# Kernel optimization log

Measured on AMD Instinct MI355X. Metric: run time of the kernel, lower is better.

Reference implementation:

```python
import jax
import jax.numpy as jnp
import numpy as np

B, R, C, Q, D = 16, 2048, 81, 65, 1024
K = 1024          # pre-NMS candidate cap (fixed-shape stand-in for torch's dynamic filtering)
DET = 100         # detections_per_img
IMG = 640.0       # square image size (clip bound)
SCORE_THRESH = 0.05
NMS_THRESH = 0.5
MIN_SIZE = 0.01
BBOX_CLIP = float(np.log(1000.0 / 16.0))  # torchvision BoxCoder bbox_xform_clip
WX, WY, WW, WH = 10.0, 10.0, 5.0, 5.0     # BoxCoder weights


def setup_inputs() -> dict:
    key = jax.random.key(0)
    k1, k2, k3, k4, k5, k6 = jax.random.split(key, 6)
    class_logits = 2.0 * jax.random.normal(k1, (B, R, C), jnp.float32)
    quantity_logits = jax.random.normal(k2, (B, R, Q), jnp.float32)
    box_features = jax.random.normal(k3, (B, R, D), jnp.float32)
    box_regression = 0.5 * jax.random.normal(k4, (B, R, C * 4), jnp.float32)
    cxcy = jax.random.uniform(k5, (B, R, 2), jnp.float32, 0.0, IMG)
    wh = jax.random.uniform(k6, (B, R, 2), jnp.float32, 10.0, 80.0)
    x1y1 = jnp.clip(cxcy - 0.5 * wh, 0.0, IMG)
    x2y2 = jnp.clip(cxcy + 0.5 * wh, 0.0, IMG)
    proposals = jnp.concatenate([x1y1, x2y2], axis=-1)
    return {
        'class_logits': class_logits,
        'quantity_logits': quantity_logits,
        'box_features': box_features,
        'box_regression': box_regression,
        'proposals': proposals,
    }


def _decode(deltas, props):
    # deltas: [R, C, 4], props: [R, 4] -> boxes [R, C, 4] (torchvision BoxCoder.decode)
    pw = props[:, 2] - props[:, 0]
    ph = props[:, 3] - props[:, 1]
    pcx = props[:, 0] + 0.5 * pw
    pcy = props[:, 1] + 0.5 * ph
    dx = deltas[..., 0] / WX
    dy = deltas[..., 1] / WY
    dw = jnp.minimum(deltas[..., 2] / WW, BBOX_CLIP)
    dh = jnp.minimum(deltas[..., 3] / WH, BBOX_CLIP)
    cx = dx * pw[:, None] + pcx[:, None]
    cy = dy * ph[:, None] + pcy[:, None]
    w = jnp.exp(dw) * pw[:, None]
    h = jnp.exp(dh) * ph[:, None]
    return jnp.stack([cx - 0.5 * w, cy - 0.5 * h, cx + 0.5 * w, cy + 0.5 * h], axis=-1)


def _iou_matrix(b):
    # b: [K, 4] -> pairwise IoU [K, K]
    area = (b[:, 2] - b[:, 0]) * (b[:, 3] - b[:, 1])
    lt = jnp.maximum(b[:, None, :2], b[None, :, :2])
    rb = jnp.minimum(b[:, None, 2:], b[None, :, 2:])
    whv = jnp.clip(rb - lt, 0.0)
    inter = whv[..., 0] * whv[..., 1]
    return inter / (area[:, None] + area[None, :] - inter + 1e-9)


def _process_image(logits, qlogits, feats, reg, props):
    # decode + clip
    boxes = jnp.clip(_decode(reg.reshape(R, C, 4), props), 0.0, IMG)  # [R, C, 4]
    scores = jax.nn.softmax(logits, axis=-1)                          # [R, C]
    quant = jnp.argmax(qlogits, axis=-1).astype(jnp.int32)            # [R]
    # drop background class 0, flatten to M = R*(C-1)
    fb = boxes[:, 1:, :].reshape(-1, 4)
    fs = scores[:, 1:].reshape(-1)
    fl = jnp.broadcast_to(jnp.arange(1, C, dtype=jnp.int32), (R, C - 1)).reshape(-1)
    fi = jnp.broadcast_to(jnp.arange(R, dtype=jnp.int32)[:, None], (R, C - 1)).reshape(-1)
    bw = fb[:, 2] - fb[:, 0]
    bh = fb[:, 3] - fb[:, 1]
    valid = (fs > SCORE_THRESH) & (bw >= MIN_SIZE) & (bh >= MIN_SIZE)
    # top-K candidates by masked score (sorted desc)
    top_s, top_i = jax.lax.top_k(jnp.where(valid, fs, -1.0), K)
    cb = fb[top_i]          # [K, 4]
    cl = fl[top_i]          # [K]
    ci = fi[top_i]          # [K] row index into proposals/features
    cv = top_s > 0.0        # candidate validity (score_thresh > 0)
    # batched NMS via per-class coordinate offset
    ob = cb + (cl.astype(jnp.float32) * (IMG + 1.0))[:, None]
    iou = _iou_matrix(ob)
    ar = jnp.arange(K)

    def body(i, keep):
        sup = (iou[i] > NMS_THRESH) & (ar > i)
        return jnp.where(keep[i] & cv[i], keep & ~sup, keep)

    keep = jax.lax.fori_loop(0, K, body, cv) & cv
    # first DET survivors in score order
    det_s, det_i = jax.lax.top_k(jnp.where(keep, top_s, -1.0), DET)
    dv = det_s > 0.0
    m = dv.astype(jnp.float32)
    db = cb[det_i] * m[:, None]
    dl = jnp.where(dv, cl[det_i], 0)
    di = ci[det_i]
    dq = jnp.where(dv, quant[di], 0)
    df = feats[di] * m[:, None]   # irregular gather of box features by surviving row idx
    ds = jnp.where(dv, det_s, 0.0)
    return db, ds, dl, dq, df, dv


def reference(class_logits, quantity_logits, box_features, box_regression, proposals):
    # returns (boxes [B,DET,4], scores [B,DET], labels [B,DET] i32,
    #          quantities [B,DET] i32, features [B,DET,D], valid [B,DET] bool)
    return jax.vmap(_process_image)(class_logits, quantity_logits, box_features,
                                    box_regression, proposals)
```

## Files before the change

### kernel.cpp

```cpp
#include <hip/hip_runtime.h>
#include <math.h>

#define NB 16
#define NR 2048
#define NC 81
#define NQ 65
#define ND 1024
#define NK 1024
#define NDET 100
#define NBLK 512
#define BSLOT 64
#define HBINS 5184
#define CH 256
#define L2CAP 384
#define LRCAP 1536
#define BBC 4.135166556742356f

#define O_BOX   0
#define O_SCORE (NB*NDET*4)
#define O_LABEL (O_SCORE + NB*NDET)
#define O_QUANT (O_LABEL + NB*NDET)
#define O_FEAT  (O_QUANT + NB*NDET)
#define O_VALID (O_FEAT + (size_t)NB*NDET*ND)

#define WS_CAND  ((size_t)0)
#define WS_GHIST (WS_CAND + (size_t)NB*NBLK*BSLOT*8)
#define WS_DETCB (WS_GHIST + (size_t)NB*HBINS*4)
#define WS_DETM  (WS_DETCB + (size_t)NB*NDET*16)
#define WS_DETS  (WS_DETM + (size_t)NB*NDET*4)
#define WS_CNT   (WS_DETS + (size_t)NB*NDET*4)

__device__ __forceinline__ float4 decode_box(float4 d, float pw, float ph,
                                             float pcx, float pcy) {
    float dx = d.x / 10.0f, dy = d.y / 10.0f;
    float dw = fminf(d.z / 5.0f, BBC), dh = fminf(d.w / 5.0f, BBC);
    float cx = dx * pw + pcx, cy = dy * ph + pcy;
    float w = expf(dw) * pw, h = expf(dh) * ph;
    float4 r;
    r.x = fminf(fmaxf(cx - 0.5f * w, 0.0f), 640.0f);
    r.y = fminf(fmaxf(cy - 0.5f * h, 0.0f), 640.0f);
    r.z = fminf(fmaxf(cx + 0.5f * w, 0.0f), 640.0f);
    r.w = fminf(fmaxf(cy + 0.5f * h, 0.0f), 640.0f);
    return r;
}

__global__ __launch_bounds__(256) void k_stage1(
    const float* __restrict__ logits, const float* __restrict__ reg,
    const float* __restrict__ props, unsigned long long* __restrict__ cand,
    int* __restrict__ cnt, unsigned int* __restrict__ ghist) {
    __shared__ unsigned long long sl[BSLOT];
    __shared__ int scnt;
    int b = blockIdx.x >> 9;
    int blk = blockIdx.x & (NBLK - 1);
    int wid = threadIdx.x >> 6;
    int lane = threadIdx.x & 63;
    int r = blk * 4 + wid;
    int row = b * NR + r;
    if (threadIdx.x == 0) scnt = 0;
    __syncthreads();

    const float* Lrow = logits + (size_t)row * NC;
    float v0 = Lrow[lane];
    float v1 = (lane < NC - 64) ? Lrow[64 + lane] : -1e30f;
    float mx = fmaxf(v0, v1);
    #pragma unroll
    for (int o = 32; o; o >>= 1) mx = fmaxf(mx, __shfl_xor(mx, o));
    float e = expf(v0 - mx) + ((lane < NC - 64) ? expf(v1 - mx) : 0.0f);
    float sm = e;
    #pragma unroll
    for (int o = 32; o; o >>= 1) sm += __shfl_xor(sm, o);
    float thr_lo = mx + logf(0.05f * sm) - 0.01f;

    const float* P = props + (size_t)row * 4;
    float p0 = P[0], p1 = P[1], p2 = P[2], p3 = P[3];
    float pw = p2 - p0, ph = p3 - p1;
    float pcx = p0 + 0.5f * pw, pcy = p1 + 0.5f * ph;
    const float* G = reg + (size_t)row * (NC * 4);

    #pragma unroll
    for (int pass = 0; pass < 2; ++pass) {
        int cc = lane + pass * 64;
        if (cc < NC - 1) {
            int c = cc + 1;
            float lc = Lrow[c];
            if (lc > thr_lo) {
                float p = expf(lc - mx) / sm;
                float4 d = *(const float4*)(G + 4 * c);
                float4 bx = decode_box(d, pw, ph, pcx, pcy);
                float bw = bx.z - bx.x, bh = bx.w - bx.y;
                if (p > 0.05f && bw >= 0.01f && bh >= 0.01f) {
                    int m = r * 80 + cc;
                    int pos = atomicAdd(&scnt, 1);
                    if (pos < BSLOT) {
                        sl[pos] = ((unsigned long long)__float_as_uint(p) << 32) |
                                  (unsigned)(~(unsigned)m);
                        unsigned bin = (__float_as_uint(p) - 0x3D000000u) >> 13;
                        atomicAdd(&ghist[b * HBINS + bin], 1u);
                    }
                }
            }
        }
    }
    __syncthreads();
    int n = scnt < BSLOT ? scnt : BSLOT;
    unsigned long long* dst = cand + ((size_t)b * NBLK + blk) * BSLOT;
    for (int i = threadIdx.x; i < n; i += 256) dst[i] = sl[i];
    if (threadIdx.x == 0) cnt[b * NBLK + blk] = n;
}

__global__ __launch_bounds__(1024) void k_fused(
    const unsigned long long* __restrict__ cand, const int* __restrict__ cnt,
    const unsigned int* __restrict__ ghist,
    const float* __restrict__ reg, const float* __restrict__ props,
    int* __restrict__ det_m, float* __restrict__ det_s,
    float4* __restrict__ det_cb) {
    __shared__ union {
        unsigned int hist[HBINS];
        unsigned long long sortedRest[LRCAP];
    } u;
    __shared__ unsigned long long list2[L2CAP], sorted2[L2CAP];
    __shared__ unsigned long long listRest[LRCAP];
    __shared__ float4 boff[L2CAP], bclip[L2CAP];
    __shared__ int scn[NBLK];
    __shared__ int s_c2, s_cR, s_b1, s_b2, s_A, s_need;
    int b = blockIdx.x, tid = threadIdx.x;
    const unsigned long long* cnd = cand + (size_t)b * NBLK * BSLOT;

    for (int i = tid; i < HBINS; i += 1024) u.hist[i] = ghist[b * HBINS + i];
    if (tid < NBLK) scn[tid] = cnt[b * NBLK + tid];
    if (tid == 0) { s_c2 = 0; s_cR = 0; s_b1 = 0; s_b2 = 0; s_A = 0; s_need = 0; }
    __syncthreads();

    if (tid < 64) {
        int lane = tid, base = lane * 81;
        unsigned partial = 0;
        for (int j = 0; j < 81; ++j) partial += u.hist[base + j];
        unsigned incl = partial;
        #pragma unroll
        for (int o = 1; o < 64; o <<= 1) {
            unsigned t = __shfl_up(incl, o);
            if (lane >= o) incl += t;
        }
        unsigned total = __shfl(incl, 63);
        unsigned suffix = total - incl;
        if (suffix < NK && suffix + partial >= NK) {
            unsigned A = suffix;
            for (int bb = base + 80; bb >= base; --bb) {
                unsigned An = A + u.hist[bb];
                if (An >= NK) { s_b1 = bb; break; }
                A = An;
            }
        }
        if (suffix < CH && suffix + partial >= CH) {
            unsigned A = suffix;
            for (int bb = base + 80; bb >= base; --bb) {
                unsigned An = A + u.hist[bb];
                if (An >= CH) { s_b2 = bb; break; }
                A = An;
            }
        }
    }
    __syncthreads();
    int b1 = s_b1, b2 = s_b2;

    for (int i = tid; i < NBLK * BSLOT; i += 1024) {
        if ((i & (BSLOT - 1)) < scn[i >> 6]) {
            unsigned long long key = cnd[i];
            int bin = (int)(((unsigned)(key >> 32) - 0x3D000000u) >> 13);
            if (bin >= b2) {
                int p = atomicAdd(&s_c2, 1);
                if (p < L2CAP) list2[p] = key;
            } else if (bin >= b1) {
                int p = atomicAdd(&s_cR, 1);
                if (p < LRCAP) listRest[p] = key;
            }
        }
    }
    __syncthreads();
    int T2 = s_c2 < L2CAP ? s_c2 : L2CAP;
    int TR = s_cR < LRCAP ? s_cR : LRCAP;
    int S = T2 + TR;
    int cap = S < NK ? S : NK;
    int limit1 = T2 < cap ? T2 : cap;

    if (tid < T2) {
        unsigned long long k0 = list2[tid];
        int rk = 0;
        for (int j = 0; j < T2; ++j) rk += (list2[j] > k0);
        sorted2[rk] = k0;
    }
    __syncthreads();

    if (tid < limit1) {
        unsigned long long key = sorted2[tid];
        int m = (int)(~(unsigned)key);
        int r = m / 80, c = m - r * 80 + 1;
        size_t row = (size_t)b * NR + r;
        float4 P = *(const float4*)(props + row * 4);
        float pw = P.z - P.x, ph = P.w - P.y;
        float pcx = P.x + 0.5f * pw, pcy = P.y + 0.5f * ph;
        float4 d = *(const float4*)(reg + row * (NC * 4) + 4 * c);
        float4 bx = decode_box(d, pw, ph, pcx, pcy);
        bclip[tid] = bx;
        float off = (float)c * 641.0f;
        float4 o = {bx.x + off, bx.y + off, bx.z + off, bx.w + off};
        boff[tid] = o;
    }
    __syncthreads();

    int lane = tid & 63;
    float4 a0 = {0, 0, 0, 0}, a1 = {0, 0, 0, 0};
    int A = 0;
    if (tid < 64) {
        unsigned long long nk_ = (limit1 > 0) ? sorted2[0] : 0ull;
        float4 nb_ = (limit1 > 0) ? boff[0] : a0;
        for (int t = 0; t < limit1; ++t) {
            unsigned long long keyt = nk_;
            float4 bt = nb_;
            if (t + 1 < limit1) { nk_ = sorted2[t + 1]; nb_ = boff[t + 1]; }
            float areaB = (bt.z - bt.x) * (bt.w - bt.y);
            float areaA0 = (a0.z - a0.x) * (a0.w - a0.y);
            float ltx = fmaxf(a0.x, bt.x), lty = fmaxf(a0.y, bt.y);
            float rbx = fminf(a0.z, bt.z), rby = fminf(a0.w, bt.w);
            float in0 = fmaxf(rbx - ltx, 0.0f) * fmaxf(rby - lty, 0.0f);
            bool sup = (lane < A) && (in0 / (areaA0 + areaB - in0 + 1e-9f) > 0.5f);
            if (A > 64) {
                float areaA1 = (a1.z - a1.x) * (a1.w - a1.y);
                float l1 = fmaxf(a1.x, bt.x), t1 = fmaxf(a1.y, bt.y);
                float r1 = fminf(a1.z, bt.z), b1f = fminf(a1.w, bt.w);
                float in1 = fmaxf(r1 - l1, 0.0f) * fmaxf(b1f - t1, 0.0f);
                sup |= (lane + 64 < A) &&
                       (in1 / (areaA1 + areaB - in1 + 1e-9f) > 0.5f);
            }
            if (!__any((int)sup)) {
                if (lane == (A & 63)) { if (A < 64) a0 = bt; else a1 = bt; }
                if (lane == 0) {
                    det_m[b * NDET + A] = (int)(~(unsigned)keyt);
                    det_s[b * NDET + A] = __uint_as_float((unsigned)(keyt >> 32));
                    det_cb[b * NDET + A] = bclip[t];
                }
                ++A;
                if (A == NDET) break;
            }
        }
        if (tid == 0) { s_A = A; s_need = (A < NDET && limit1 < cap) ? 1 : 0; }
    }
    __syncthreads();

    if (s_need) {
        for (int t0 = tid; t0 < TR; t0 += 1024) {
            unsigned long long k0 = listRest[t0];
            int rk = 0;
            for (int j = 0; j < TR; ++j) rk += (listRest[j] > k0);
            u.sortedRest[rk] = k0;
        }
        __syncthreads();
        if (tid < 64) {
            int nrest = cap - limit1;
            for (int t = 0; t < nrest && A < NDET; ++t) {
                unsigned long long keyt = u.sortedRest[t];
                int m = (int)(~(unsigned)keyt);
                int r = m / 80, c = m - r * 80 + 1;
                size_t row = (size_t)b * NR + r;
                float4 P = *(const float4*)(props + row * 4);
                float pw = P.z - P.x, ph = P.w - P.y;
                float pcx = P.x + 0.5f * pw, pcy = P.y + 0.5f * ph;
                float4 d = *(const float4*)(reg + row * (NC * 4) + 4 * c);
                float4 bx = decode_box(d, pw, ph, pcx, pcy);
                float off = (float)c * 641.0f;
                float4 bt = {bx.x + off, bx.y + off, bx.z + off, bx.w + off};
                float areaB = (bt.z - bt.x) * (bt.w - bt.y);
                float areaA0 = (a0.z - a0.x) * (a0.w - a0.y);
                float ltx = fmaxf(a0.x, bt.x), lty = fmaxf(a0.y, bt.y);
                float rbx = fminf(a0.z, bt.z), rby = fminf(a0.w, bt.w);
                float in0 = fmaxf(rbx - ltx, 0.0f) * fmaxf(rby - lty, 0.0f);
                bool sup = (lane < A) &&
                           (in0 / (areaA0 + areaB - in0 + 1e-9f) > 0.5f);
                if (A > 64) {
                    float areaA1 = (a1.z - a1.x) * (a1.w - a1.y);
                    float l1 = fmaxf(a1.x, bt.x), t1 = fmaxf(a1.y, bt.y);
                    float r1 = fminf(a1.z, bt.z), b1f = fminf(a1.w, bt.w);
                    float in1 = fmaxf(r1 - l1, 0.0f) * fmaxf(b1f - t1, 0.0f);
                    sup |= (lane + 64 < A) &&
                           (in1 / (areaA1 + areaB - in1 + 1e-9f) > 0.5f);
                }
                if (!__any((int)sup)) {
                    if (lane == (A & 63)) { if (A < 64) a0 = bt; else a1 = bt; }
                    if (lane == 0) {
                        det_m[b * NDET + A] = m;
                        det_s[b * NDET + A] =
                            __uint_as_float((unsigned)(keyt >> 32));
                        det_cb[b * NDET + A] = bx;
                    }
                    ++A;
                }
            }
            if (tid == 0) s_A = A;
        }
        __syncthreads();
    }
    for (int d = s_A + tid; d < NDET; d += 1024) det_m[b * NDET + d] = -1;
}

__global__ __launch_bounds__(256) void k_final(
    const float* __restrict__ feats, const float* __restrict__ qlog,
    const int* __restrict__ det_m, const float* __restrict__ det_s,
    const float4* __restrict__ det_cb, float* __restrict__ out) {
    int bd = blockIdx.x;
    int b = bd / NDET;
    int t = threadIdx.x;
    int m = det_m[bd];
    float4* of = (float4*)(out + O_FEAT + (size_t)bd * ND);
    if (m >= 0) {
        int r = m / 80, c = m - r * 80 + 1;
        size_t row = (size_t)b * NR + r;
        if (t == 0) {
            ((float4*)(out + O_BOX))[bd] = det_cb[bd];
            out[O_SCORE + bd] = det_s[bd];
            out[O_LABEL + bd] = (float)c;
            out[O_VALID + bd] = 1.0f;
        }
        if (t < 64) {
            const float* Qrow = qlog + row * NQ;
            float qv = Qrow[t];
            int qi = t;
            if (t == 0) {
                float q64 = Qrow[64];
                if (q64 > qv) { qv = q64; qi = 64; }
            }
            #pragma unroll
            for (int o = 32; o; o >>= 1) {
                float ov = __shfl_xor(qv, o);
                int oi = __shfl_xor(qi, o);
                if (ov > qv || (ov == qv && oi < qi)) { qv = ov; qi = oi; }
            }
            if (t == 0) out[O_QUANT + bd] = (float)qi;
        }
        const float4* f = (const float4*)(feats + row * ND);
        of[t] = f[t];
    } else {
        if (t == 0) {
            float4 z = {0, 0, 0, 0};
            ((float4*)(out + O_BOX))[bd] = z;
            out[O_SCORE + bd] = 0.0f;
            out[O_LABEL + bd] = 0.0f;
            out[O_QUANT + bd] = 0.0f;
            out[O_VALID + bd] = 0.0f;
        }
        float4 z = {0, 0, 0, 0};
        of[t] = z;
    }
}

extern "C" void kernel_launch(void* const* d_in, const int* in_sizes, int n_in,
                              void* d_out, int out_size, void* d_ws, size_t ws_size,
                              hipStream_t stream) {
    const float* logits = (const float*)d_in[0];
    const float* qlog   = (const float*)d_in[1];
    const float* feats  = (const float*)d_in[2];
    const float* reg    = (const float*)d_in[3];
    const float* props  = (const float*)d_in[4];
    float* out = (float*)d_out;
    char* ws = (char*)d_ws;

    unsigned long long* cand = (unsigned long long*)(ws + WS_CAND);
    unsigned int* ghist = (unsigned int*)(ws + WS_GHIST);
    float4* det_cb = (float4*)(ws + WS_DETCB);
    int* det_m = (int*)(ws + WS_DETM);
    float* det_s = (float*)(ws + WS_DETS);
    int* cnt = (int*)(ws + WS_CNT);

    hipMemsetAsync(ghist, 0, (size_t)NB * HBINS * 4, stream);
    k_stage1<<<NB * NBLK, 256, 0, stream>>>(logits, reg, props, cand, cnt, ghist);
    k_fused<<<NB, 1024, 0, stream>>>(cand, cnt, ghist, reg, props, det_m, det_s,
                                     det_cb);
    k_final<<<NB * NDET, 256, 0, stream>>>(feats, qlog, det_m, det_s, det_cb, out);
}
```

Baseline: 294.8 us.

## Fuse all stages into one cooperative persistent kernel with grid syncs

Replaces the memset plus three kernel launches with a single cooperative kernel of 512 blocks that uses grid.sync between histogram clearing, candidate scoring, per-image NMS and output gathering. Stage 1 now assigns 16 rows per wave and compacts candidates with ballot/popcount into per-wave slots instead of shared-memory atomics. The aim is to remove launch and inter-kernel gaps. In exchange, the NMS stage runs on only 16 blocks of 256 threads, down from 1024, while the other blocks sit idle at a grid barrier, and the scoring phase has less parallelism.

```diff
diff --git a/kernel.cpp b/kernel.cpp
--- a/kernel.cpp
+++ b/kernel.cpp
@@ -1,5 +1,8 @@
 #include <hip/hip_runtime.h>
+#include <hip/hip_cooperative_groups.h>
 #include <math.h>
+
+namespace cg = cooperative_groups;
 
 #define NB 16
 #define NR 2048
@@ -8,8 +11,11 @@
 #define ND 1024
 #define NK 1024
 #define NDET 100
-#define NBLK 512
-#define BSLOT 64
+#define GRID 512
+#define NWAVE 2048
+#define WPI 128
+#define RPW 16
+#define WSLOT 128
 #define HBINS 5184
 #define CH 256
 #define L2CAP 384
@@ -24,11 +30,11 @@
 #define O_VALID (O_FEAT + (size_t)NB*NDET*ND)
 
 #define WS_CAND  ((size_t)0)
-#define WS_GHIST (WS_CAND + (size_t)NB*NBLK*BSLOT*8)
-#define WS_DETCB (WS_GHIST + (size_t)NB*HBINS*4)
-#define WS_DETM  (WS_DETCB + (size_t)NB*NDET*16)
+#define WS_GHIST (WS_CAND + (size_t)NWAVE*WSLOT*8)
+#define WS_CNT   (WS_GHIST + (size_t)NB*HBINS*4)
+#define WS_DETM  (WS_CNT + (size_t)NWAVE*4)
 #define WS_DETS  (WS_DETM + (size_t)NB*NDET*4)
-#define WS_CNT   (WS_DETS + (size_t)NB*NDET*4)
+#define WS_DETCB (WS_DETS + (size_t)NB*NDET*4)
 
 __device__ __forceinline__ float4 decode_box(float4 d, float pw, float ph,
                                              float pcx, float pcy) {
@@ -44,231 +50,191 @@
     return r;
 }
 
-__global__ __launch_bounds__(256) void k_stage1(
-    const float* __restrict__ logits, const float* __restrict__ reg,
-    const float* __restrict__ props, unsigned long long* __restrict__ cand,
-    int* __restrict__ cnt, unsigned int* __restrict__ ghist) {
-    __shared__ unsigned long long sl[BSLOT];
-    __shared__ int scnt;
-    int b = blockIdx.x >> 9;
-    int blk = blockIdx.x & (NBLK - 1);
-    int wid = threadIdx.x >> 6;
-    int lane = threadIdx.x & 63;
-    int r = blk * 4 + wid;
-    int row = b * NR + r;
-    if (threadIdx.x == 0) scnt = 0;
-    __syncthreads();
-
-    const float* Lrow = logits + (size_t)row * NC;
-    float v0 = Lrow[lane];
-    float v1 = (lane < NC - 64) ? Lrow[64 + lane] : -1e30f;
-    float mx = fmaxf(v0, v1);
-    #pragma unroll
-    for (int o = 32; o; o >>= 1) mx = fmaxf(mx, __shfl_xor(mx, o));
-    float e = expf(v0 - mx) + ((lane < NC - 64) ? expf(v1 - mx) : 0.0f);
-    float sm = e;
-    #pragma unroll
-    for (int o = 32; o; o >>= 1) sm += __shfl_xor(sm, o);
-    float thr_lo = mx + logf(0.05f * sm) - 0.01f;
-
-    const float* P = props + (size_t)row * 4;
-    float p0 = P[0], p1 = P[1], p2 = P[2], p3 = P[3];
-    float pw = p2 - p0, ph = p3 - p1;
-    float pcx = p0 + 0.5f * pw, pcy = p1 + 0.5f * ph;
-    const float* G = reg + (size_t)row * (NC * 4);
-
-    #pragma unroll
-    for (int pass = 0; pass < 2; ++pass) {
-        int cc = lane + pass * 64;
-        if (cc < NC - 1) {
-            int c = cc + 1;
-            float lc = Lrow[c];
-            if (lc > thr_lo) {
-                float p = expf(lc - mx) / sm;
-                float4 d = *(const float4*)(G + 4 * c);
-                float4 bx = decode_box(d, pw, ph, pcx, pcy);
-                float bw = bx.z - bx.x, bh = bx.w - bx.y;
-                if (p > 0.05f && bw >= 0.01f && bh >= 0.01f) {
-                    int m = r * 80 + cc;
-                    int pos = atomicAdd(&scnt, 1);
-                    if (pos < BSLOT) {
-                        sl[pos] = ((unsigned long long)__float_as_uint(p) << 32) |
-                                  (unsigned)(~(unsigned)m);
-                        unsigned bin = (__float_as_uint(p) - 0x3D000000u) >> 13;
-                        atomicAdd(&ghist[b * HBINS + bin], 1u);
-                    }
-                }
-            }
-        }
-    }
-    __syncthreads();
-    int n = scnt < BSLOT ? scnt : BSLOT;
-    unsigned long long* dst = cand + ((size_t)b * NBLK + blk) * BSLOT;
-    for (int i = threadIdx.x; i < n; i += 256) dst[i] = sl[i];
-    if (threadIdx.x == 0) cnt[b * NBLK + blk] = n;
-}
-
-__global__ __launch_bounds__(1024) void k_fused(
-    const unsigned long long* __restrict__ cand, const int* __restrict__ cnt,
-    const unsigned int* __restrict__ ghist,
-    const float* __restrict__ reg, const float* __restrict__ props,
-    int* __restrict__ det_m, float* __restrict__ det_s,
-    float4* __restrict__ det_cb) {
-    __shared__ union {
+struct SharedB {
+    union {
         unsigned int hist[HBINS];
         unsigned long long sortedRest[LRCAP];
     } u;
-    __shared__ unsigned long long list2[L2CAP], sorted2[L2CAP];
-    __shared__ unsigned long long listRest[LRCAP];
-    __shared__ float4 boff[L2CAP], bclip[L2CAP];
-    __shared__ int scn[NBLK];
-    __shared__ int s_c2, s_cR, s_b1, s_b2, s_A, s_need;
-    int b = blockIdx.x, tid = threadIdx.x;
-    const unsigned long long* cnd = cand + (size_t)b * NBLK * BSLOT;
-
-    for (int i = tid; i < HBINS; i += 1024) u.hist[i] = ghist[b * HBINS + i];
-    if (tid < NBLK) scn[tid] = cnt[b * NBLK + tid];
-    if (tid == 0) { s_c2 = 0; s_cR = 0; s_b1 = 0; s_b2 = 0; s_A = 0; s_need = 0; }
-    __syncthreads();
-
-    if (tid < 64) {
-        int lane = tid, base = lane * 81;
-        unsigned partial = 0;
-        for (int j = 0; j < 81; ++j) partial += u.hist[base + j];
-        unsigned incl = partial;
-        #pragma unroll
-        for (int o = 1; o < 64; o <<= 1) {
-            unsigned t = __shfl_up(incl, o);
-            if (lane >= o) incl += t;
-        }
-        unsigned total = __shfl(incl, 63);
-        unsigned suffix = total - incl;
-        if (suffix < NK && suffix + partial >= NK) {
-            unsigned A = suffix;
-            for (int bb = base + 80; bb >= base; --bb) {
-                unsigned An = A + u.hist[bb];
-                if (An >= NK) { s_b1 = bb; break; }
-                A = An;
-            }
-        }
-        if (suffix < CH && suffix + partial >= CH) {
-            unsigned A = suffix;
-            for (int bb = base + 80; bb >= base; --bb) {
-                unsigned An = A + u.hist[bb];
-                if (An >= CH) { s_b2 = bb; break; }
-                A = An;
-            }
-        }
+    unsigned long long list2[L2CAP], sorted2[L2CAP], listRest[LRCAP];
+    float4 boff[L2CAP], bclip[L2CAP];
+    int scn[WPI];
+    int s_c2, s_cR, s_b1, s_b2, s_A, s_need;
+};
+
+__global__ __launch_bounds__(256, 2) void k_all(
+    const float* __restrict__ logits, const float* __restrict__ qlog,
+    const float* __restrict__ feats, const float* __restrict__ reg,
+    const float* __restrict__ props, unsigned long long* __restrict__ cand,
+    unsigned int* __restrict__ ghist, int* __restrict__ cnt,
+    int* __restrict__ det_m, float* __restrict__ det_s,
+    float4* __restrict__ det_cb, float* __restrict__ out) {
+    cg::grid_group grid = cg::this_grid();
+    __shared__ SharedB sb;
+    int tid = threadIdx.x;
+    int lane = tid & 63;
+
+    for (int i = blockIdx.x * 256 + tid; i < NB * HBINS; i += GRID * 256)
+        ghist[i] = 0;
+    grid.sync();
+
+    {
+        int W = blockIdx.x * 4 + (tid >> 6);
+        int b = W >> 7, wi = W & (WPI - 1);
+        unsigned long long* wreg = cand + (size_t)W * WSLOT;
+        int cur = 0;
+        for (int t = 0; t < RPW; ++t) {
+            int r = wi * RPW + t;
+            int row = b * NR + r;
+            const float* Lrow = logits + (size_t)row * NC;
+            float v0 = Lrow[lane];
+            float v1 = (lane < NC - 64) ? Lrow[64 + lane] : -1e30f;
+            float mx = fmaxf(v0, v1);
+            #pragma unroll
+            for (int o = 32; o; o >>= 1) mx = fmaxf(mx, __shfl_xor(mx, o));
+            float e = expf(v0 - mx) + ((lane < NC - 64) ? expf(v1 - mx) : 0.0f);
+            float sm = e;
+            #pragma unroll
+            for (int o = 32; o; o >>= 1) sm += __shfl_xor(sm, o);
+            float thr_lo = mx + logf(0.05f * sm) - 0.01f;
+
+            float4 P = *(const float4*)(props + (size_t)row * 4);
+            float pw = P.z - P.x, ph = P.w - P.y;
+            float pcx = P.x + 0.5f * pw, pcy = P.y + 0.5f * ph;
+            const float* G = reg + (size_t)row * (NC * 4);
+
+            #pragma unroll
+            for (int pass = 0; pass < 2; ++pass) {
+                int cc = lane + pass * 64;
+                bool ok = false;
+                unsigned long long key = 0;
+                if (cc < NC - 1) {
+                    int c = cc + 1;
+                    float lc = Lrow[c];
+                    if (lc > thr_lo) {
+                        float p = expf(lc - mx) / sm;
+                        float4 d = *(const float4*)(G + 4 * c);
+                        float4 bx = decode_box(d, pw, ph, pcx, pcy);
+                        float bw = bx.z - bx.x, bh = bx.w - bx.y;
+                        if (p > 0.05f && bw >= 0.01f && bh >= 0.01f) {
+                            ok = true;
+                            unsigned m = (unsigned)(r * 80 + cc);
+                            key = ((unsigned long long)__float_as_uint(p) << 32) |
+                                  (unsigned)(~m);
+                        }
+                    }
+                }
+                unsigned long long msk = __ballot(ok);
+                int rk = __popcll(msk & ((1ull << lane) - 1ull));
+                if (ok && cur + rk < WSLOT) {
+                    wreg[cur + rk] = key;
+                    unsigned bin = ((unsigned)(key >> 32) - 0x3D000000u) >> 13;
+                    atomicAdd(&ghist[b * HBINS + bin], 1u);
+                }
+                cur += (int)__popcll(msk);
+            }
+        }
+        if (lane == 0) cnt[W] = cur < WSLOT ? cur : WSLOT;
     }
-    __syncthreads();
-    int b1 = s_b1, b2 = s_b2;
-
-    for (int i = tid; i < NBLK * BSLOT; i += 1024) {
-        if ((i & (BSLOT - 1)) < scn[i >> 6]) {
-            unsigned long long key = cnd[i];
-            int bin = (int)(((unsigned)(key >> 32) - 0x3D000000u) >> 13);
-            if (bin >= b2) {
-                int p = atomicAdd(&s_c2, 1);
-                if (p < L2CAP) list2[p] = key;
-            } else if (bin >= b1) {
-                int p = atomicAdd(&s_cR, 1);
-                if (p < LRCAP) listRest[p] = key;
-            }
-        }
-    }
-    __syncthreads();
-    int T2 = s_c2 < L2CAP ? s_c2 : L2CAP;
-    int TR = s_cR < LRCAP ? s_cR : LRCAP;
-    int S = T2 + TR;
-    int cap = S < NK ? S : NK;
-    int limit1 = T2 < cap ? T2 : cap;
-
-    if (tid < T2) {
-        unsigned long long k0 = list2[tid];
-        int rk = 0;
-        for (int j = 0; j < T2; ++j) rk += (list2[j] > k0);
-        sorted2[rk] = k0;
-    }
-    __syncthreads();
-
-    if (tid < limit1) {
-        unsigned long long key = sorted2[tid];
-        int m = (int)(~(unsigned)key);
-        int r = m / 80, c = m - r * 80 + 1;
-        size_t row = (size_t)b * NR + r;
-        float4 P = *(const float4*)(props + row * 4);
-        float pw = P.z - P.x, ph = P.w - P.y;
-        float pcx = P.x + 0.5f * pw, pcy = P.y + 0.5f * ph;
-        float4 d = *(const float4*)(reg + row * (NC * 4) + 4 * c);
-        float4 bx = decode_box(d, pw, ph, pcx, pcy);
-        bclip[tid] = bx;
-        float off = (float)c * 641.0f;
-        float4 o = {bx.x + off, bx.y + off, bx.z + off, bx.w + off};
-        boff[tid] = o;
-    }
-    __syncthreads();
-
-    int lane = tid & 63;
-    float4 a0 = {0, 0, 0, 0}, a1 = {0, 0, 0, 0};
-    int A = 0;
-    if (tid < 64) {
-        unsigned long long nk_ = (limit1 > 0) ? sorted2[0] : 0ull;
-        float4 nb_ = (limit1 > 0) ? boff[0] : a0;
-        for (int t = 0; t < limit1; ++t) {
-            unsigned long long keyt = nk_;
-            float4 bt = nb_;
-            if (t + 1 < limit1) { nk_ = sorted2[t + 1]; nb_ = boff[t + 1]; }
-            float areaB = (bt.z - bt.x) * (bt.w - bt.y);
-            float areaA0 = (a0.z - a0.x) * (a0.w - a0.y);
-            float ltx = fmaxf(a0.x, bt.x), lty = fmaxf(a0.y, bt.y);
-            float rbx = fminf(a0.z, bt.z), rby = fminf(a0.w, bt.w);
-            float in0 = fmaxf(rbx - ltx, 0.0f) * fmaxf(rby - lty, 0.0f);
-            bool sup = (lane < A) && (in0 / (areaA0 + areaB - in0 + 1e-9f) > 0.5f);
-            if (A > 64) {
-                float areaA1 = (a1.z - a1.x) * (a1.w - a1.y);
-                float l1 = fmaxf(a1.x, bt.x), t1 = fmaxf(a1.y, bt.y);
-                float r1 = fminf(a1.z, bt.z), b1f = fminf(a1.w, bt.w);
-                float in1 = fmaxf(r1 - l1, 0.0f) * fmaxf(b1f - t1, 0.0f);
-                sup |= (lane + 64 < A) &&
-                       (in1 / (areaA1 + areaB - in1 + 1e-9f) > 0.5f);
-            }
-            if (!__any((int)sup)) {
-                if (lane == (A & 63)) { if (A < 64) a0 = bt; else a1 = bt; }
-                if (lane == 0) {
-                    det_m[b * NDET + A] = (int)(~(unsigned)keyt);
-                    det_s[b * NDET + A] = __uint_as_float((unsigned)(keyt >> 32));
-                    det_cb[b * NDET + A] = bclip[t];
-                }
-                ++A;
-                if (A == NDET) break;
-            }
-        }
-        if (tid == 0) { s_A = A; s_need = (A < NDET && limit1 < cap) ? 1 : 0; }
-    }
-    __syncthreads();
-
-    if (s_need) {
-        for (int t0 = tid; t0 < TR; t0 += 1024) {
-            unsigned long long k0 = listRest[t0];
+    grid.sync();
+
+    if (blockIdx.x < NB) {
+        int b = blockIdx.x;
+        const unsigned long long* cnd = cand + (size_t)b * WPI * WSLOT;
+
+        for (int i = tid; i < HBINS; i += 256) sb.u.hist[i] = ghist[b * HBINS + i];
+        if (tid < WPI) sb.scn[tid] = cnt[b * WPI + tid];
+        if (tid == 0) {
+            sb.s_c2 = 0; sb.s_cR = 0; sb.s_b1 = 0; sb.s_b2 = 0;
+            sb.s_A = 0; sb.s_need = 0;
+        }
+        __syncthreads();
+
+        if (tid < 64) {
+            int base = lane * 81;
+            unsigned partial = 0;
+            for (int j = 0; j < 81; ++j) partial += sb.u.hist[base + j];
+            unsigned incl = partial;
+            #pragma unroll
+            for (int o = 1; o < 64; o <<= 1) {
+                unsigned t = __shfl_up(incl, o);
+                if (lane >= o) incl += t;
+            }
+            unsigned total = __shfl(incl, 63);
+            unsigned suffix = total - incl;
+            if (suffix < NK && suffix + partial >= NK) {
+                unsigned A = suffix;
+                for (int bb = base + 80; bb >= base; --bb) {
+                    unsigned An = A + sb.u.hist[bb];
+                    if (An >= NK) { sb.s_b1 = bb; break; }
+                    A = An;
+                }
+            }
+            if (suffix < CH && suffix + partial >= CH) {
+                unsigned A = suffix;
+                for (int bb = base + 80; bb >= base; --bb) {
+                    unsigned An = A + sb.u.hist[bb];
+                    if (An >= CH) { sb.s_b2 = bb; break; }
+                    A = An;
+                }
+            }
+        }
+        __syncthreads();
+        int b1 = sb.s_b1, b2 = sb.s_b2;
+
+        for (int i = tid; i < WPI * WSLOT; i += 256) {
+            if ((i & (WSLOT - 1)) < sb.scn[i >> 7]) {
+                unsigned long long key = cnd[i];
+                int bin = (int)(((unsigned)(key >> 32) - 0x3D000000u) >> 13);
+                if (bin >= b2) {
+                    int p = atomicAdd(&sb.s_c2, 1);
+                    if (p < L2CAP) sb.list2[p] = key;
+                } else if (bin >= b1) {
+                    int p = atomicAdd(&sb.s_cR, 1);
+                    if (p < LRCAP) sb.listRest[p] = key;
+                }
+            }
+        }
+        __syncthreads();
+        int T2 = sb.s_c2 < L2CAP ? sb.s_c2 : L2CAP;
+        int TR = sb.s_cR < LRCAP ? sb.s_cR : LRCAP;
+        int S = T2 + TR;
+        int cap = S < NK ? S : NK;
+        int limit1 = T2 < cap ? T2 : cap;
+
+        for (int t0 = tid; t0 < T2; t0 += 256) {
+            unsigned long long k0 = sb.list2[t0];
             int rk = 0;
-            for (int j = 0; j < TR; ++j) rk += (listRest[j] > k0);
-            u.sortedRest[rk] = k0;
-        }
-        __syncthreads();
+            for (int j = 0; j < T2; ++j) rk += (sb.list2[j] > k0);
+            sb.sorted2[rk] = k0;
+        }
+        __syncthreads();
+
+        for (int t0 = tid; t0 < limit1; t0 += 256) {
+            unsigned long long key = sb.sorted2[t0];
+            int m = (int)(~(unsigned)key);
+            int r = m / 80, c = m - r * 80 + 1;
+            size_t row = (size_t)b * NR + r;
+            float4 P = *(const float4*)(props + row * 4);
+            float pw = P.z - P.x, ph = P.w - P.y;
+            float pcx = P.x + 0.5f * pw, pcy = P.y + 0.5f * ph;
+            float4 d = *(const float4*)(reg + row * (NC * 4) + 4 * c);
+            float4 bx = decode_box(d, pw, ph, pcx, pcy);
+            sb.bclip[t0] = bx;
+            float off = (float)c * 641.0f;
+            float4 o = {bx.x + off, bx.y + off, bx.z + off, bx.w + off};
+            sb.boff[t0] = o;
+        }
+        __syncthreads();
+
+        float4 a0 = {0, 0, 0, 0}, a1 = {0, 0, 0, 0};
+        int A = 0;
         if (tid < 64) {
-            int nrest = cap - limit1;
-            for (int t = 0; t < nrest && A < NDET; ++t) {
-                unsigned long long keyt = u.sortedRest[t];
-                int m = (int)(~(unsigned)keyt);
-                int r = m / 80, c = m - r * 80 + 1;
-                size_t row = (size_t)b * NR + r;
-                float4 P = *(const float4*)(props + row * 4);
-                float pw = P.z - P.x, ph = P.w - P.y;
-                float pcx = P.x + 0.5f * pw, pcy = P.y + 0.5f * ph;
-                float4 d = *(const float4*)(reg + row * (NC * 4) + 4 * c);
-                float4 bx = decode_box(d, pw, ph, pcx, pcy);
-                float off = (float)c * 641.0f;
-                float4 bt = {bx.x + off, bx.y + off, bx.z + off, bx.w + off};
+            unsigned long long nk_ = (limit1 > 0) ? sb.sorted2[0] : 0ull;
+            float4 nb_ = (limit1 > 0) ? sb.boff[0] : a0;
+            for (int t = 0; t < limit1; ++t) {
+                unsigned long long keyt = nk_;
+                float4 bt = nb_;
+                if (t + 1 < limit1) { nk_ = sb.sorted2[t + 1]; nb_ = sb.boff[t + 1]; }
                 float areaB = (bt.z - bt.x) * (bt.w - bt.y);
                 float areaA0 = (a0.z - a0.x) * (a0.w - a0.y);
                 float ltx = fmaxf(a0.x, bt.x), lty = fmaxf(a0.y, bt.y);
@@ -287,68 +253,121 @@
                 if (!__any((int)sup)) {
                     if (lane == (A & 63)) { if (A < 64) a0 = bt; else a1 = bt; }
                     if (lane == 0) {
-                        det_m[b * NDET + A] = m;
+                        det_m[b * NDET + A] = (int)(~(unsigned)keyt);
                         det_s[b * NDET + A] =
                             __uint_as_float((unsigned)(keyt >> 32));
-                        det_cb[b * NDET + A] = bx;
+                        det_cb[b * NDET + A] = sb.bclip[t];
                     }
                     ++A;
-                }
-            }
-            if (tid == 0) s_A = A;
-        }
-        __syncthreads();
+                    if (A == NDET) break;
+                }
+            }
+            if (tid == 0) {
+                sb.s_A = A;
+                sb.s_need = (A < NDET && limit1 < cap) ? 1 : 0;
+            }
+        }
+        __syncthreads();
+
+        if (sb.s_need) {
+            for (int t0 = tid; t0 < TR; t0 += 256) {
+                unsigned long long k0 = sb.listRest[t0];
+                int rk = 0;
+                for (int j = 0; j < TR; ++j) rk += (sb.listRest[j] > k0);
+                sb.u.sortedRest[rk] = k0;
+            }
+            __syncthreads();
+            if (tid < 64) {
+                int nrest = cap - limit1;
+                for (int t = 0; t < nrest && A < NDET; ++t) {
+                    unsigned long long keyt = sb.u.sortedRest[t];
+                    int m = (int)(~(unsigned)keyt);
+                    int r = m / 80, c = m - r * 80 + 1;
+                    size_t row = (size_t)b * NR + r;
+                    float4 P = *(const float4*)(props + row * 4);
+                    float pw = P.z - P.x, ph = P.w - P.y;
+                    float pcx = P.x + 0.5f * pw, pcy = P.y + 0.5f * ph;
+                    float4 d = *(const float4*)(reg + row * (NC * 4) + 4 * c);
+                    float4 bx = decode_box(d, pw, ph, pcx, pcy);
+                    float off = (float)c * 641.0f;
+                    float4 bt = {bx.x + off, bx.y + off, bx.z + off, bx.w + off};
+                    float areaB = (bt.z - bt.x) * (bt.w - bt.y);
+                    float areaA0 = (a0.z - a0.x) * (a0.w - a0.y);
+                    float ltx = fmaxf(a0.x, bt.x), lty = fmaxf(a0.y, bt.y);
+                    float rbx = fminf(a0.z, bt.z), rby = fminf(a0.w, bt.w);
+                    float in0 = fmaxf(rbx - ltx, 0.0f) * fmaxf(rby - lty, 0.0f);
+                    bool sup = (lane < A) &&
+                               (in0 / (areaA0 + areaB - in0 + 1e-9f) > 0.5f);
+                    if (A > 64) {
+                        float areaA1 = (a1.z - a1.x) * (a1.w - a1.y);
+                        float l1 = fmaxf(a1.x, bt.x), t1 = fmaxf(a1.y, bt.y);
+                        float r1 = fminf(a1.z, bt.z), b1f = fminf(a1.w, bt.w);
+                        float in1 = fmaxf(r1 - l1, 0.0f) * fmaxf(b1f - t1, 0.0f);
+                        sup |= (lane + 64 < A) &&
+                               (in1 / (areaA1 + areaB - in1 + 1e-9f) > 0.5f);
+                    }
+                    if (!__any((int)sup)) {
+                        if (lane == (A & 63)) { if (A < 64) a0 = bt; else a1 = bt; }
+                        if (lane == 0) {
+                            det_m[b * NDET + A] = m;
+                            det_s[b * NDET + A] =
+                                __uint_as_float((unsigned)(keyt >> 32));
+                            det_cb[b * NDET + A] = bx;
+                        }
+                        ++A;
+                    }
+                }
+                if (tid == 0) sb.s_A = A;
+            }
+            __syncthreads();
+        }
+        for (int d = sb.s_A + tid; d < NDET; d += 256) det_m[b * NDET + d] = -1;
     }
-    for (int d = s_A + tid; d < NDET; d += 1024) det_m[b * NDET + d] = -1;
-}
-
-__global__ __launch_bounds__(256) void k_final(
-    const float* __restrict__ feats, const float* __restrict__ qlog,
-    const int* __restrict__ det_m, const float* __restrict__ det_s,
-    const float4* __restrict__ det_cb, float* __restrict__ out) {
-    int bd = blockIdx.x;
-    int b = bd / NDET;
-    int t = threadIdx.x;
-    int m = det_m[bd];
-    float4* of = (float4*)(out + O_FEAT + (size_t)bd * ND);
-    if (m >= 0) {
-        int r = m / 80, c = m - r * 80 + 1;
-        size_t row = (size_t)b * NR + r;
-        if (t == 0) {
-            ((float4*)(out + O_BOX))[bd] = det_cb[bd];
-            out[O_SCORE + bd] = det_s[bd];
-            out[O_LABEL + bd] = (float)c;
-            out[O_VALID + bd] = 1.0f;
-        }
-        if (t < 64) {
-            const float* Qrow = qlog + row * NQ;
-            float qv = Qrow[t];
-            int qi = t;
-            if (t == 0) {
-                float q64 = Qrow[64];
-                if (q64 > qv) { qv = q64; qi = 64; }
-            }
-            #pragma unroll
-            for (int o = 32; o; o >>= 1) {
-                float ov = __shfl_xor(qv, o);
-                int oi = __shfl_xor(qi, o);
-                if (ov > qv || (ov == qv && oi < qi)) { qv = ov; qi = oi; }
-            }
-            if (t == 0) out[O_QUANT + bd] = (float)qi;
-        }
-        const float4* f = (const float4*)(feats + row * ND);
-        of[t] = f[t];
-    } else {
-        if (t == 0) {
+    grid.sync();
+
+    for (int bd = blockIdx.x; bd < NB * NDET; bd += GRID) {
+        int b = bd / NDET;
+        int m = det_m[bd];
+        float4* of = (float4*)(out + O_FEAT + (size_t)bd * ND);
+        if (m >= 0) {
+            int r = m / 80, c = m - r * 80 + 1;
+            size_t row = (size_t)b * NR + r;
+            if (tid == 0) {
+                ((float4*)(out + O_BOX))[bd] = det_cb[bd];
+                out[O_SCORE + bd] = det_s[bd];
+                out[O_LABEL + bd] = (float)c;
+                out[O_VALID + bd] = 1.0f;
+            }
+            if (tid < 64) {
+                const float* Qrow = qlog + row * NQ;
+                float qv = Qrow[lane];
+                int qi = lane;
+                if (lane == 0) {
+                    float q64 = Qrow[64];
+                    if (q64 > qv) { qv = q64; qi = 64; }
+                }
+                #pragma unroll
+                for (int o = 32; o; o >>= 1) {
+                    float ov = __shfl_xor(qv, o);
+                    int oi = __shfl_xor(qi, o);
+                    if (ov > qv || (ov == qv && oi < qi)) { qv = ov; qi = oi; }
+                }
+                if (lane == 0) out[O_QUANT + bd] = (float)qi;
+            }
+            const float4* f = (const float4*)(feats + row * ND);
+            of[tid] = f[tid];
+        } else {
+            if (tid == 0) {
+                float4 z = {0, 0, 0, 0};
+                ((float4*)(out + O_BOX))[bd] = z;
+                out[O_SCORE + bd] = 0.0f;
+                out[O_LABEL + bd] = 0.0f;
+                out[O_QUANT + bd] = 0.0f;
+                out[O_VALID + bd] = 0.0f;
+            }
             float4 z = {0, 0, 0, 0};
-            ((float4*)(out + O_BOX))[bd] = z;
-            out[O_SCORE + bd] = 0.0f;
-            out[O_LABEL + bd] = 0.0f;
-            out[O_QUANT + bd] = 0.0f;
-            out[O_VALID + bd] = 0.0f;
-        }
-        float4 z = {0, 0, 0, 0};
-        of[t] = z;
+            of[tid] = z;
+        }
     }
 }
 
@@ -365,14 +384,14 @@
 
     unsigned long long* cand = (unsigned long long*)(ws + WS_CAND);
     unsigned int* ghist = (unsigned int*)(ws + WS_GHIST);
-    float4* det_cb = (float4*)(ws + WS_DETCB);
+    int* cnt = (int*)(ws + WS_CNT);
     int* det_m = (int*)(ws + WS_DETM);
     float* det_s = (float*)(ws + WS_DETS);
-    int* cnt = (int*)(ws + WS_CNT);
-
-    hipMemsetAsync(ghist, 0, (size_t)NB * HBINS * 4, stream);
-    k_stage1<<<NB * NBLK, 256, 0, stream>>>(logits, reg, props, cand, cnt, ghist);
-    k_fused<<<NB, 1024, 0, stream>>>(cand, cnt, ghist, reg, props, det_m, det_s,
-                                     det_cb);
-    k_final<<<NB * NDET, 256, 0, stream>>>(feats, qlog, det_m, det_s, det_cb, out);
+    float4* det_cb = (float4*)(ws + WS_DETCB);
+
+    void* args[] = {(void*)&logits, (void*)&qlog, (void*)&feats, (void*)&reg,
+                    (void*)&props, (void*)&cand, (void*)&ghist, (void*)&cnt,
+                    (void*)&det_m, (void*)&det_s, (void*)&det_cb, (void*)&out};
+    hipLaunchCooperativeKernel((void*)k_all, dim3(GRID), dim3(256), args, 0,
+                               stream);
 }
```

After: 487.0 us. 65.2% more time.
